# Performance work log

Measured on AMD Instinct MI355X. Metric: run time of the kernel, lower is better.

The kernel has to match this reference:

```python
import jax, jax.numpy as jnp
import numpy as np

G = 3040      # number of drugs / graph nodes in the drug-drug graph
A = 100       # atoms per molecular graph (smileNode, uniform)
TOK = 43      # token vocabulary (hard-coded in module)
FS = 75       # nfeat_smile
HS = 128      # nhid_smile
H1S = 128     # nhid1_smile
NF = 512      # nfeat (raw 384 + 128 smile emb)
NH = 256      # nhid
DH = 256      # dhid1


def setup_inputs() -> dict:
    key = jax.random.key(0)
    ks = jax.random.split(key, 20)
    s = 0.05
    inp = {
        "x": jax.random.normal(ks[0], (G, NF - H1S), dtype=jnp.float32),
        "adj_pos": jax.random.uniform(ks[1], (G, G), dtype=jnp.float32) / G,
        "adj_neg": jax.random.uniform(ks[2], (G, G), dtype=jnp.float32) / G,
        "mol_adj": jax.random.uniform(ks[3], (G, A, A), dtype=jnp.float32) / A,
        "encoded_drug": jax.random.randint(ks[4], (G, A), 0, TOK, dtype=jnp.int64),
        # learned params
        "tok_emb": jax.random.normal(ks[5], (TOK, FS), dtype=jnp.float32),
        "Wm1": jax.random.normal(ks[6], (G, FS, HS), dtype=jnp.float32) * s,
        "Wm2": jax.random.normal(ks[7], (G, HS, H1S), dtype=jnp.float32) * s,
        "Wp1": jax.random.normal(ks[8], (NF, NH), dtype=jnp.float32) * s,
        "Wp2": jax.random.normal(ks[9], (NH, NH), dtype=jnp.float32) * s,
        "Wn1": jax.random.normal(ks[10], (NF, NH), dtype=jnp.float32) * s,
        "Wn2": jax.random.normal(ks[11], (NH, NH), dtype=jnp.float32) * s,
        "Wd1": jax.random.normal(ks[12], (2 * NH, DH), dtype=jnp.float32) * s,
        "Wd2": jax.random.normal(ks[13], (DH, 2 * DH), dtype=jnp.float32) * s,
        "Wd3": jax.random.normal(ks[14], (2 * DH, DH), dtype=jnp.float32) * s,
        "Wdec": jax.random.normal(ks[15], (DH, DH), dtype=jnp.float32) * s,
    }
    return inp


def reference(x, adj_pos, adj_neg, mol_adj, encoded_drug, tok_emb,
              Wm1, Wm2, Wp1, Wp2, Wn1, Wn2, Wd1, Wd2, Wd3, Wdec):
    # --- calDrugSmileFeatures: batched over all 3040 per-graph GCN encoders ---
    feats = tok_emb[encoded_drug]                          # [G, A, FS] (embedding gather)
    h = jnp.einsum('gab,gaf,gfh->gbh', mol_adj, feats, Wm1)  # gc1: adj @ (x @ W1), per graph
    h = jnp.einsum('gab,gah,ghk->gbk', mol_adj, h, Wm2)      # gc2 (dropout inactive, eval)
    emb_drugs = jnp.max(h, axis=1)                          # [G, H1S] node-wise maxpool

    # --- main drug-drug graph ---
    xc = jnp.concatenate([x, emb_drugs], axis=1)            # [G, NF]
    hp = jax.nn.relu(adj_pos @ (xc @ Wp1))                  # GCNEncoder pos layer1
    zp = adj_pos @ (hp @ Wp2)                               # layer2
    hn = jax.nn.relu(adj_neg @ (xc @ Wn1))
    zn = adj_neg @ (hn @ Wn2)
    z = jnp.concatenate([zp, zn], axis=1)                   # [G, 2*NH]

    # --- DSN MLP (eval: dropout inactive) ---
    z = jax.nn.relu(z @ Wd1)
    z = jax.nn.relu(z @ Wd2)
    z = z @ Wd3                                             # [G, DH]

    # --- Bilinear decoder: z W z^T logits ---
    y_pred = (z @ Wdec) @ z.T                               # [G, G]
    return y_pred
```

## Files before the change

kernel.cpp:

```cpp
#include <hip/hip_runtime.h>
#include <cstdint>
#include <cstddef>

#define Gn   3040
#define An   100
#define TOKn 43
#define FSn  75
#define NFn  512
#define XC   384

typedef __attribute__((ext_vector_type(8))) short s16x8;
typedef __attribute__((ext_vector_type(4))) float f32x4;

__device__ __forceinline__ void split_bf16(float x, unsigned short &h, unsigned short &l)
{
  unsigned u = __float_as_uint(x);
  unsigned r = (u + 0x7fffu + ((u >> 16) & 1u)) & 0xffff0000u;
  h = (unsigned short)(r >> 16);
  float res = x - __uint_as_float(r);
  unsigned v = __float_as_uint(res);
  l = (unsigned short)((v + 0x7fffu + ((v >> 16) & 1u)) >> 16);
}

#define MFMA3(acc, ah, al, bh, bl)                                              \
  acc = __builtin_amdgcn_mfma_f32_16x16x32_bf16(ah, bh, acc, 0, 0, 0);          \
  acc = __builtin_amdgcn_mfma_f32_16x16x32_bf16(ah, bl, acc, 0, 0, 0);          \
  acc = __builtin_amdgcn_mfma_f32_16x16x32_bf16(al, bh, acc, 0, 0, 0);

__device__ __forceinline__ s16x8 tail_frag(const unsigned short* p, bool act)
{
  s16x8 f = {0,0,0,0,0,0,0,0};
  if (act) {
    uint2 v = *(const uint2*)p;
    f[0] = (short)(v.x & 0xffffu); f[1] = (short)(v.x >> 16);
    f[2] = (short)(v.y & 0xffffu); f[3] = (short)(v.y >> 16);
  }
  return f;
}

__device__ __forceinline__ void pack_split4(const f32x4 a, uint2 &ph, uint2 &pl)
{
  unsigned short h[4], l[4];
  #pragma unroll
  for (int r = 0; r < 4; ++r) split_bf16(a[r], h[r], l[r]);
  ph.x = (unsigned)h[0] | ((unsigned)h[1] << 16);
  ph.y = (unsigned)h[2] | ((unsigned)h[3] << 16);
  pl.x = (unsigned)l[0] | ((unsigned)l[1] << 16);
  pl.y = (unsigned)l[2] | ((unsigned)l[3] << 16);
}

__global__ void prep_tok_kernel(const float* __restrict__ tok_emb,
                                unsigned short* __restrict__ th,
                                unsigned short* __restrict__ tl)
{
  int i = blockIdx.x * 256 + threadIdx.x;
  if (i >= TOKn * 96) return;
  int r = i / 96, f = i % 96;
  float v = (f < FSn) ? tok_emb[r * FSn + f] : 0.f;
  unsigned short h, l;
  split_bf16(v, h, l);
  th[i] = h; tl[i] = l;
}

__global__ __launch_bounds__(512, 1) void smile_mfma_kernel(
    const float* __restrict__ mol_adj, const int* __restrict__ enc,
    const unsigned short* __restrict__ tokh, const unsigned short* __restrict__ tokl,
    const float* __restrict__ Wm1, const float* __restrict__ Wm2,
    float* __restrict__ xc)
{
  __shared__ __align__(16) unsigned short sm[74624];
  __shared__ int sTok[An];
  unsigned short* adjT_h = sm;
  unsigned short* adjT_l = sm + 10400;
  unsigned short* bufA_h = sm + 20800;
  unsigned short* bufA_l = sm + 34112;
  unsigned short* g1_h   = sm + 47424;
  unsigned short* g1_l   = sm + 61024;

  const int g = blockIdx.x;
  const int t = threadIdx.x;
  const int w = t >> 6, l = t & 63;
  const int lr = l & 15, lq = l >> 4;
  const f32x4 z4 = {0.f, 0.f, 0.f, 0.f};
  const s16x8 z8 = {0,0,0,0,0,0,0,0};

  if (t < An) sTok[t] = enc[g * An + t];

  {
    const float* adjg = mol_adj + (size_t)g * (An * An);
    for (int i = t; i < 2500; i += 512) {
      const int a = i / 25, b4 = (i % 25) * 4;
      float4 v = *(const float4*)&adjg[i * 4];
      unsigned short hh, ll;
      split_bf16(v.x, hh, ll); adjT_h[(b4+0)*104 + a] = hh; adjT_l[(b4+0)*104 + a] = ll;
      split_bf16(v.y, hh, ll); adjT_h[(b4+1)*104 + a] = hh; adjT_l[(b4+1)*104 + a] = ll;
      split_bf16(v.z, hh, ll); adjT_h[(b4+2)*104 + a] = hh; adjT_l[(b4+2)*104 + a] = ll;
      split_bf16(v.w, hh, ll); adjT_h[(b4+3)*104 + a] = hh; adjT_l[(b4+3)*104 + a] = ll;
    }
  }
  __syncthreads();

  {
    const int h = 16 * w + lr;
    const float* W1 = Wm1 + (size_t)g * (FSn * 128);
    s16x8 bh[3], bl[3];
    #pragma unroll
    for (int kc = 0; kc < 3; ++kc) {
      #pragma unroll
      for (int j = 0; j < 8; ++j) {
        int f = 32 * kc + 8 * lq + j;
        float v = (f < FSn) ? W1[f * 128 + h] : 0.f;
        unsigned short hh, ll;
        split_bf16(v, hh, ll);
        bh[kc][j] = (short)hh; bl[kc][j] = (short)ll;
      }
    }
    f32x4 acc[7];
    #pragma unroll
    for (int mi = 0; mi < 7; ++mi) acc[mi] = z4;
    #pragma unroll
    for (int mi = 0; mi < 7; ++mi) {
      const int a = 16 * mi + lr;
      const bool va = a < An;
      const int tk = va ? sTok[a] : 0;
      const unsigned short* th = tokh + tk * 96 + 8 * lq;
      const unsigned short* tl = tokl + tk * 96 + 8 * lq;
      #pragma unroll
      for (int kc = 0; kc < 3; ++kc) {
        s16x8 ah = z8, al = z8;
        if (va) { ah = *(const s16x8*)&th[32 * kc]; al = *(const s16x8*)&tl[32 * kc]; }
        MFMA3(acc[mi], ah, al, bh[kc], bl[kc]);
      }
    }
    #pragma unroll
    for (int mi = 0; mi < 7; ++mi) {
      const int a0 = 16 * mi + 4 * lq;
      if (a0 < An) {
        uint2 ph, pl;
        pack_split4(acc[mi], ph, pl);
        *(uint2*)&bufA_h[h * 104 + a0] = ph;
        *(uint2*)&bufA_l[h * 104 + a0] = pl;
      }
    }
  }
  __syncthreads();

  {
    const unsigned short* xh = &bufA_h[(16 * w + lr) * 104];
    const unsigned short* xl = &bufA_l[(16 * w + lr) * 104];
    f32x4 acc[7];
    #pragma unroll
    for (int ni = 0; ni < 7; ++ni) acc[ni] = z4;
    #pragma unroll
    for (int kc = 0; kc < 4; ++kc) {
      s16x8 ah, al;
      if (kc < 3) {
        ah = *(const s16x8*)&xh[32 * kc + 8 * lq];
        al = *(const s16x8*)&xl[32 * kc + 8 * lq];
      } else {
        ah = tail_frag(xh + 96, lq == 0);
        al = tail_frag(xl + 96, lq == 0);
      }
      #pragma unroll
      for (int ni = 0; ni < 7; ++ni) {
        const int b = 16 * ni + lr;
        const bool vb = b < An;
        s16x8 bh = z8, bl = z8;
        if (kc < 3) {
          if (vb) {
            bh = *(const s16x8*)&adjT_h[b * 104 + 32 * kc + 8 * lq];
            bl = *(const s16x8*)&adjT_l[b * 104 + 32 * kc + 8 * lq];
          }
        } else {
          bh = tail_frag(&adjT_h[b * 104 + 96], vb && lq == 0);
          bl = tail_frag(&adjT_l[b * 104 + 96], vb && lq == 0);
        }
        MFMA3(acc[ni], ah, al, bh, bl);
      }
    }
    __syncthreads();
    #pragma unroll
    for (int ni = 0; ni < 7; ++ni) {
      const int b = 16 * ni + lr;
      if (b < An) {
        uint2 ph, pl;
        pack_split4(acc[ni], ph, pl);
        *(uint2*)&g1_h[b * 136 + 16 * w + 4 * lq] = ph;
        *(uint2*)&g1_l[b * 136 + 16 * w + 4 * lq] = pl;
      }
    }
  }
  __syncthreads();

  {
    const int k2 = 16 * w + lr;
    const float* W2 = Wm2 + (size_t)g * (128 * 128);
    s16x8 bh[4], bl[4];
    #pragma unroll
    for (int kc = 0; kc < 4; ++kc) {
      #pragma unroll
      for (int j = 0; j < 8; ++j) {
        float v = W2[(32 * kc + 8 * lq + j) * 128 + k2];
        unsigned short hh, ll;
        split_bf16(v, hh, ll);
        bh[kc][j] = (short)hh; bl[kc][j] = (short)ll;
      }
    }
    f32x4 acc[7];
    #pragma unroll
    for (int mi = 0; mi < 7; ++mi) acc[mi] = z4;
    #pragma unroll
    for (int kc = 0; kc < 4; ++kc) {
      #pragma unroll
      for (int mi = 0; mi < 7; ++mi) {
        const int b = 16 * mi + lr;
        const bool vb = b < An;
        s16x8 ah = z8, al = z8;
        if (vb) {
          ah = *(const s16x8*)&g1_h[b * 136 + 32 * kc + 8 * lq];
          al = *(const s16x8*)&g1_l[b * 136 + 32 * kc + 8 * lq];
        }
        MFMA3(acc[mi], ah, al, bh[kc], bl[kc]);
      }
    }
    __syncthreads();
    #pragma unroll
    for (int mi = 0; mi < 7; ++mi) {
      const int b0 = 16 * mi + 4 * lq;
      if (b0 < An) {
        uint2 ph, pl;
        pack_split4(acc[mi], ph, pl);
        *(uint2*)&bufA_h[k2 * 104 + b0] = ph;
        *(uint2*)&bufA_l[k2 * 104 + b0] = pl;
      }
    }
  }
  __syncthreads();

  {
    const unsigned short* fh = &bufA_h[(16 * w + lr) * 104];
    const unsigned short* fl = &bufA_l[(16 * w + lr) * 104];
    f32x4 acc[7];
    #pragma unroll
    for (int ni = 0; ni < 7; ++ni) acc[ni] = z4;
    #pragma unroll
    for (int kc = 0; kc < 4; ++kc) {
      s16x8 ah, al;
      if (kc < 3) {
        ah = *(const s16x8*)&fh[32 * kc + 8 * lq];
        al = *(const s16x8*)&fl[32 * kc + 8 * lq];
      } else {
        ah = tail_frag(fh + 96, lq == 0);
        al = tail_frag(fl + 96, lq == 0);
      }
      #pragma unroll
      for (int ni = 0; ni < 7; ++ni) {
        const int b = 16 * ni + lr;
        const bool vb = b < An;
        s16x8 bh = z8, bl = z8;
        if (kc < 3) {
          if (vb) {
            bh = *(const s16x8*)&adjT_h[b * 104 + 32 * kc + 8 * lq];
            bl = *(const s16x8*)&adjT_l[b * 104 + 32 * kc + 8 * lq];
          }
        } else {
          bh = tail_frag(&adjT_h[b * 104 + 96], vb && lq == 0);
          bl = tail_frag(&adjT_l[b * 104 + 96], vb && lq == 0);
        }
        MFMA3(acc[ni], ah, al, bh, bl);
      }
    }
    float mr[4] = {-3.4e38f, -3.4e38f, -3.4e38f, -3.4e38f};
    #pragma unroll
    for (int ni = 0; ni < 7; ++ni) {
      if (16 * ni + lr < An) {
        #pragma unroll
        for (int r = 0; r < 4; ++r) mr[r] = fmaxf(mr[r], acc[ni][r]);
      }
    }
    #pragma unroll
    for (int d = 1; d < 16; d <<= 1) {
      #pragma unroll
      for (int r = 0; r < 4; ++r) mr[r] = fmaxf(mr[r], __shfl_xor(mr[r], d, 64));
    }
    if (lr == 0) {
      const int k2b = 16 * w + 4 * lq;
      #pragma unroll
      for (int r = 0; r < 4; ++r)
        xc[(size_t)g * NFn + XC + k2b + r] = mr[r];
    }
  }
}

__global__ __launch_bounds__(256, 2) void gemm64_kernel(
    const float* __restrict__ A0, const float* __restrict__ A1,
    const float* __restrict__ B0, const float* __restrict__ B1,
    float* __restrict__ C0, float* __restrict__ C1,
    int M, int N, int K, int relu)
{
  const float* A = blockIdx.z ? A1 : A0;
  const float* B = blockIdx.z ? B1 : B0;
  float*       C = blockIdx.z ? C1 : C0;

  __shared__ float As[16][68];
  __shared__ float Bs[16][68];

  const int t  = threadIdx.x;
  const int m0 = blockIdx.x * 64, n0 = blockIdx.y * 64;
  const int tx = t & 15, ty = t >> 4;
  const int am = t >> 2,  ak = (t & 3) * 4;
  const int bk = t >> 4,  bn = (t & 15) * 4;

  float acc[4][4];
  #pragma unroll
  for (int i = 0; i < 4; ++i)
    #pragma unroll
    for (int j = 0; j < 4; ++j) acc[i][j] = 0.f;

  for (int k0 = 0; k0 < K; k0 += 16) {
    float4 av = make_float4(0.f, 0.f, 0.f, 0.f);
    if (m0 + am < M) av = *(const float4*)&A[(size_t)(m0 + am) * K + k0 + ak];
    float4 bv = *(const float4*)&B[(size_t)(k0 + bk) * N + n0 + bn];
    __syncthreads();
    As[ak + 0][am] = av.x; As[ak + 1][am] = av.y;
    As[ak + 2][am] = av.z; As[ak + 3][am] = av.w;
    *(float4*)&Bs[bk][bn] = bv;
    __syncthreads();
    #pragma unroll
    for (int kk = 0; kk < 16; ++kk) {
      float4 a4 = *(const float4*)&As[kk][ty * 4];
      float4 b4 = *(const float4*)&Bs[kk][tx * 4];
      const float aa[4] = {a4.x, a4.y, a4.z, a4.w};
      const float bb[4] = {b4.x, b4.y, b4.z, b4.w};
      #pragma unroll
      for (int i = 0; i < 4; ++i)
        #pragma unroll
        for (int j = 0; j < 4; ++j)
          acc[i][j] = fmaf(aa[i], bb[j], acc[i][j]);
    }
  }
  #pragma unroll
  for (int i = 0; i < 4; ++i) {
    int m = m0 + ty * 4 + i;
    if (m < M) {
      float4 v = make_float4(acc[i][0], acc[i][1], acc[i][2], acc[i][3]);
      if (relu) {
        v.x = fmaxf(v.x, 0.f); v.y = fmaxf(v.y, 0.f);
        v.z = fmaxf(v.z, 0.f); v.w = fmaxf(v.w, 0.f);
      }
      *(float4*)&C[(size_t)m * N + n0 + tx * 4] = v;
    }
  }
}

__global__ __launch_bounds__(256) void convT_kernel(
    const float* __restrict__ S0, const float* __restrict__ S1,
    unsigned short* __restrict__ H0, unsigned short* __restrict__ L0,
    unsigned short* __restrict__ H1, unsigned short* __restrict__ L1)
{
  __shared__ float sT[32][33];
  const float* S     = blockIdx.z ? S1 : S0;
  unsigned short* H  = blockIdx.z ? H1 : H0;
  unsigned short* Lo = blockIdx.z ? L1 : L0;
  const int t  = threadIdx.x;
  const int r0 = blockIdx.x * 32;
  const int c0 = blockIdx.y * 32;
  {
    const int i = t >> 3, j0 = (t & 7) * 4;
    float4 v = *(const float4*)&S[(size_t)(r0 + i) * 256 + c0 + j0];
    sT[i][j0] = v.x; sT[i][j0+1] = v.y; sT[i][j0+2] = v.z; sT[i][j0+3] = v.w;
  }
  __syncthreads();
  {
    const int jj = t >> 3, ii0 = (t & 7) * 4;
    unsigned short h[4], lo[4];
    #pragma unroll
    for (int q = 0; q < 4; ++q) split_bf16(sT[ii0 + q][jj], h[q], lo[q]);
    ushort4 hv = make_ushort4(h[0], h[1], h[2], h[3]);
    ushort4 lv = make_ushort4(lo[0], lo[1], lo[2], lo[3]);
    *(ushort4*)&H [(size_t)(c0 + jj) * Gn + r0 + ii0] = hv;
    *(ushort4*)&Lo[(size_t)(c0 + jj) * Gn + r0 + ii0] = lv;
  }
}

template<bool SPLIT, bool BF32>
__global__ __launch_bounds__(256, 2) void mgemm_kernel(
    const float* __restrict__ A0, const float* __restrict__ A1,
    const unsigned short* __restrict__ Bh0, const unsigned short* __restrict__ Bl0,
    const unsigned short* __restrict__ Bh1, const unsigned short* __restrict__ Bl1,
    const float* __restrict__ Bf,
    float* __restrict__ C0, float* __restrict__ C1,
    int M, int N, int K)
{
  __shared__ __align__(16) unsigned short lds[16384];

  const int z = blockIdx.z;
  int pair, k0base, kend;
  if (SPLIT) {
    pair = z & 1;
    int s = z >> 1;
    k0base = s * 768;
    kend = k0base + 768; if (kend > K) kend = K;
  } else { pair = 0; k0base = 0; kend = K; }

  const float* A = pair ? A1 : A0;
  const unsigned short* Bh = pair ? Bh1 : Bh0;
  const unsigned short* Bl = pair ? Bl1 : Bl0;
  float* C;
  if (SPLIT) C = (pair ? C1 : C0) + (size_t)(z >> 1) * M * N;
  else       C = C0;

  const int t  = threadIdx.x;
  const int l  = t & 63;
  const int wv = t >> 6;
  const int wr = wv >> 1, wc = wv & 1;
  const int m0 = blockIdx.x * 128, n0 = blockIdx.y * 128;

  const int sm = (t >> 6) * 16 + (t & 15);
  const int sk = ((t >> 4) & 3) * 8;

  const f32x4 zero4 = {0.f, 0.f, 0.f, 0.f};
  f32x4 acc[4][4];
  #pragma unroll
  for (int i = 0; i < 4; ++i)
    #pragma unroll
    for (int j = 0; j < 4; ++j) acc[i][j] = zero4;

  for (int k0 = k0base; k0 < kend; k0 += 32) {
    float4 a00 = make_float4(0.f,0.f,0.f,0.f), a01 = a00, a10 = a00, a11 = a00;
    {
      const size_t base = (size_t)(m0 + sm) * K + k0 + sk;
      if (m0 + sm < M)      { a00 = *(const float4*)&A[base];
                              a01 = *(const float4*)&A[base + 4]; }
      if (m0 + sm + 64 < M) { a10 = *(const float4*)&A[base + (size_t)64 * K];
                              a11 = *(const float4*)&A[base + (size_t)64 * K + 4]; }
    }
    s16x8 b0h, b0l, b1h, b1l;
    float4 bf00, bf01, bf10, bf11;
    if (BF32) {
      bf00 = make_float4(0.f,0.f,0.f,0.f); bf01 = bf00; bf10 = bf00; bf11 = bf00;
      const size_t base = (size_t)(n0 + sm) * K + k0 + sk;
      if (n0 + sm < N)      { bf00 = *(const float4*)&Bf[base];
                              bf01 = *(const float4*)&Bf[base + 4]; }
      if (n0 + sm + 64 < N) { bf10 = *(const float4*)&Bf[base + (size_t)64 * K];
                              bf11 = *(const float4*)&Bf[base + (size_t)64 * K + 4]; }
    } else {
      const size_t base = (size_t)(n0 + sm) * K + k0 + sk;
      b0h = *(const s16x8*)&Bh[base];
      b0l = *(const s16x8*)&Bl[base];
      b1h = *(const s16x8*)&Bh[base + (size_t)64 * K];
      b1l = *(const s16x8*)&Bl[base + (size_t)64 * K];
    }

    s16x8 a0h, a0l, a1h, a1l;
    {
      const float av0[8] = {a00.x,a00.y,a00.z,a00.w,a01.x,a01.y,a01.z,a01.w};
      const float av1[8] = {a10.x,a10.y,a10.z,a10.w,a11.x,a11.y,a11.z,a11.w};
      #pragma unroll
      for (int j = 0; j < 8; ++j) {
        unsigned short hh, ll;
        split_bf16(av0[j], hh, ll); a0h[j] = (short)hh; a0l[j] = (short)ll;
        split_bf16(av1[j], hh, ll); a1h[j] = (short)hh; a1l[j] = (short)ll;
      }
    }
    if (BF32) {
      const float bv0[8] = {bf00.x,bf00.y,bf00.z,bf00.w,bf01.x,bf01.y,bf01.z,bf01.w};
      const float bv1[8] = {bf10.x,bf10.y,bf10.z,bf10.w,bf11.x,bf11.y,bf11.z,bf11.w};
      #pragma unroll
      for (int j = 0; j < 8; ++j) {
        unsigned short hh, ll;
        split_bf16(bv0[j], hh, ll); b0h[j] = (short)hh; b0l[j] = (short)ll;
        split_bf16(bv1[j], hh, ll); b1h[j] = (short)hh; b1l[j] = (short)ll;
      }
    }

    __syncthreads();
    {
      const int sl = (t & 63) * 8;
      const int c1 = t >> 6, c2 = c1 + 4;
      *(s16x8*)&lds[c1 * 512 + sl]          = a0h;
      *(s16x8*)&lds[4096 + c1 * 512 + sl]   = a0l;
      *(s16x8*)&lds[c2 * 512 + sl]          = a1h;
      *(s16x8*)&lds[4096 + c2 * 512 + sl]   = a1l;
      *(s16x8*)&lds[8192  + c1 * 512 + sl]  = b0h;
      *(s16x8*)&lds[12288 + c1 * 512 + sl]  = b0l;
      *(s16x8*)&lds[8192  + c2 * 512 + sl]  = b1h;
      *(s16x8*)&lds[12288 + c2 * 512 + sl]  = b1l;
    }
    __syncthreads();

    s16x8 vbh[4], vbl[4];
    #pragma unroll
    for (int ni = 0; ni < 4; ++ni) {
      const int c = wc * 4 + ni;
      vbh[ni] = *(const s16x8*)&lds[8192  + c * 512 + l * 8];
      vbl[ni] = *(const s16x8*)&lds[12288 + c * 512 + l * 8];
    }
    #pragma unroll
    for (int mi = 0; mi < 4; ++mi) {
      const int c = wr * 4 + mi;
      s16x8 ah = *(const s16x8*)&lds[c * 512 + l * 8];
      s16x8 al = *(const s16x8*)&lds[4096 + c * 512 + l * 8];
      #pragma unroll
      for (int ni = 0; ni < 4; ++ni) {
        acc[mi][ni] = __builtin_amdgcn_mfma_f32_16x16x32_bf16(ah, vbh[ni], acc[mi][ni], 0, 0, 0);
        acc[mi][ni] = __builtin_amdgcn_mfma_f32_16x16x32_bf16(ah, vbl[ni], acc[mi][ni], 0, 0, 0);
        acc[mi][ni] = __builtin_amdgcn_mfma_f32_16x16x32_bf16(al, vbh[ni], acc[mi][ni], 0, 0, 0);
      }
    }
  }

  #pragma unroll
  for (int mi = 0; mi < 4; ++mi) {
    const int rowb = m0 + (wr * 4 + mi) * 16 + (l >> 4) * 4;
    #pragma unroll
    for (int ni = 0; ni < 4; ++ni) {
      const int col = n0 + (wc * 4 + ni) * 16 + (l & 15);
      if (col < N) {
        #pragma unroll
        for (int r = 0; r < 4; ++r) {
          const int row = rowb + r;
          if (row < M) C[(size_t)row * N + col] = acc[mi][ni][r];
        }
      }
    }
  }
}

__global__ void reduce_kernel(const float* __restrict__ part, float* __restrict__ dst,
                              int S, int M, int N, int ldc, int coff, int relu)
{
  int i = blockIdx.x * blockDim.x + threadIdx.x;
  int total = M * (N / 4);
  if (i >= total) return;
  int r = i / (N / 4), c = (i % (N / 4)) * 4;
  float4 s = make_float4(0.f, 0.f, 0.f, 0.f);
  for (int j = 0; j < S; ++j) {
    float4 v = *(const float4*)&part[(size_t)j * M * N + (size_t)r * N + c];
    s.x += v.x; s.y += v.y; s.z += v.z; s.w += v.w;
  }
  if (relu) {
    s.x = fmaxf(s.x, 0.f); s.y = fmaxf(s.y, 0.f);
    s.z = fmaxf(s.z, 0.f); s.w = fmaxf(s.w, 0.f);
  }
  *(float4*)&dst[(size_t)r * ldc + coff + c] = s;
}

__global__ void copyx_kernel(const float* __restrict__ x, float* __restrict__ xc)
{
  int i = blockIdx.x * blockDim.x + threadIdx.x;
  int total = Gn * (XC / 4);
  if (i >= total) return;
  int r = i / (XC / 4), c = (i % (XC / 4)) * 4;
  *(float4*)&xc[(size_t)r * NFn + c] = *(const float4*)&x[(size_t)r * XC + c];
}

extern "C" void kernel_launch(void* const* d_in, const int* in_sizes, int n_in,
                              void* d_out, int out_size, void* d_ws, size_t ws_size,
                              hipStream_t stream)
{
  const float* x       = (const float*)d_in[0];
  const float* adj_pos = (const float*)d_in[1];
  const float* adj_neg = (const float*)d_in[2];
  const float* mol_adj = (const float*)d_in[3];
  const int*   enc     = (const int*)d_in[4];
  const float* tok_emb = (const float*)d_in[5];
  const float* Wm1     = (const float*)d_in[6];
  const float* Wm2     = (const float*)d_in[7];
  const float* Wp1     = (const float*)d_in[8];
  const float* Wp2     = (const float*)d_in[9];
  const float* Wn1     = (const float*)d_in[10];
  const float* Wn2     = (const float*)d_in[11];
  const float* Wd1     = (const float*)d_in[12];
  const float* Wd2     = (const float*)d_in[13];
  const float* Wd3     = (const float*)d_in[14];
  const float* Wdec    = (const float*)d_in[15];
  float* out = (float*)d_out;
  float* ws  = (float*)d_ws;

  const size_t MN  = (size_t)Gn * 256;
  const size_t MN2 = (size_t)Gn * 512;
  size_t o = 0;
  float* xc    = ws + o; o += MN2;
  float* P1    = ws + o; o += MN;
  float* N1    = ws + o; o += MN;
  float* hp    = ws + o; o += MN;
  float* hn    = ws + o; o += MN;
  float* P2    = ws + o; o += MN;
  float* N2    = ws + o; o += MN;
  float* zbuf  = ws + o; o += MN2;
  float* d1    = ws + o; o += MN;
  float* d2    = ws + o; o += MN2;
  float* z3    = ws + o; o += MN;
  float* tb    = ws + o; o += MN;
  float* partP = ws + o; o += 4 * MN;
  float* partN = ws + o; o += 4 * MN;
  unsigned short* tokh = (unsigned short*)(ws + o);
  unsigned short* tokl = tokh + TOKn * 96; o += 4128;

  unsigned short* BTPh = (unsigned short*)d2;
  unsigned short* BTPl = BTPh + (size_t)256 * Gn;
  unsigned short* BTNh = BTPh + (size_t)2 * 256 * Gn;
  unsigned short* BTNl = BTPh + (size_t)3 * 256 * Gn;

  dim3 b256(256);

  prep_tok_kernel<<<dim3((TOKn * 96 + 255) / 256), b256, 0, stream>>>(tok_emb, tokh, tokl);
  copyx_kernel<<<dim3((Gn * (XC / 4) + 255) / 256), b256, 0, stream>>>(x, xc);
  smile_mfma_kernel<<<dim3(Gn), dim3(512), 0, stream>>>(
      mol_adj, enc, tokh, tokl, Wm1, Wm2, xc);
  gemm64_kernel<<<dim3(48, 4, 2), b256, 0, stream>>>(xc, xc, Wp1, Wn1, P1, N1, Gn, 256, 512, 0);
  convT_kernel<<<dim3(95, 8, 2), b256, 0, stream>>>(P1, N1, BTPh, BTPl, BTNh, BTNl);
  mgemm_kernel<true, false><<<dim3(24, 2, 8), b256, 0, stream>>>(
      adj_pos, adj_neg, BTPh, BTPl, BTNh, BTNl, (const float*)nullptr,
      partP, partN, Gn, 256, Gn);
  reduce_kernel<<<dim3(760), b256, 0, stream>>>(partP, hp, 4, Gn, 256, 256, 0, 1);
  reduce_kernel<<<dim3(760), b256, 0, stream>>>(partN, hn, 4, Gn, 256, 256, 0, 1);
  gemm64_kernel<<<dim3(48, 4, 2), b256, 0, stream>>>(hp, hn, Wp2, Wn2, P2, N2, Gn, 256, 256, 0);
  convT_kernel<<<dim3(95, 8, 2), b256, 0, stream>>>(P2, N2, BTPh, BTPl, BTNh, BTNl);
  mgemm_kernel<true, false><<<dim3(24, 2, 8), b256, 0, stream>>>(
      adj_pos, adj_neg, BTPh, BTPl, BTNh, BTNl, (const float*)nullptr,
      partP, partN, Gn, 256, Gn);
  reduce_kernel<<<dim3(760), b256, 0, stream>>>(partP, zbuf, 4, Gn, 256, 512, 0, 0);
  reduce_kernel<<<dim3(760), b256, 0, stream>>>(partN, zbuf, 4, Gn, 256, 512, 256, 0);
  gemm64_kernel<<<dim3(48, 4, 1), b256, 0, stream>>>(zbuf, zbuf, Wd1, Wd1, d1, d1, Gn, 256, 512, 1);
  gemm64_kernel<<<dim3(48, 8, 1), b256, 0, stream>>>(d1, d1, Wd2, Wd2, d2, d2, Gn, 512, 256, 1);
  gemm64_kernel<<<dim3(48, 4, 1), b256, 0, stream>>>(d2, d2, Wd3, Wd3, z3, z3, Gn, 256, 512, 0);
  gemm64_kernel<<<dim3(48, 4, 1), b256, 0, stream>>>(z3, z3, Wdec, Wdec, tb, tb, Gn, 256, 256, 0);
  mgemm_kernel<false, true><<<dim3(24, 24, 1), b256, 0, stream>>>(
      tb, tb, (const unsigned short*)nullptr, (const unsigned short*)nullptr,
      (const unsigned short*)nullptr, (const unsigned short*)nullptr,
      z3, out, out, Gn, Gn, 256);
}
```

Before: 975.3 us.

## Prefetch all per-graph global loads upfront and transpose adjacency via LDS staging

```diff
diff --git a/kernel.cpp b/kernel.cpp
--- a/kernel.cpp
+++ b/kernel.cpp
@@ -69,13 +69,13 @@
     float* __restrict__ xc)
 {
   __shared__ __align__(16) unsigned short sm[74624];
-  __shared__ int sTok[An];
   unsigned short* adjT_h = sm;
   unsigned short* adjT_l = sm + 10400;
   unsigned short* bufA_h = sm + 20800;
   unsigned short* bufA_l = sm + 34112;
   unsigned short* g1_h   = sm + 47424;
   unsigned short* g1_l   = sm + 61024;
+  float* Sf = (float*)(sm + 20800);
 
   const int g = blockIdx.x;
   const int t = threadIdx.x;
@@ -84,51 +84,86 @@
   const f32x4 z4 = {0.f, 0.f, 0.f, 0.f};
   const s16x8 z8 = {0,0,0,0,0,0,0,0};
 
-  if (t < An) sTok[t] = enc[g * An + t];
+  const float* adjg = mol_adj + (size_t)g * (An * An);
+  float4 av[5];
+  #pragma unroll
+  for (int j = 0; j < 5; ++j) {
+    const int i = t + 512 * j;
+    av[j] = make_float4(0.f, 0.f, 0.f, 0.f);
+    if (i < 2500) av[j] = *(const float4*)&adjg[i * 4];
+  }
+  const int hcol = 16 * w + lr;
+  const float* W1 = Wm1 + (size_t)g * (FSn * 128);
+  float w1r[3][8];
+  #pragma unroll
+  for (int kc = 0; kc < 3; ++kc)
+    #pragma unroll
+    for (int j = 0; j < 8; ++j) {
+      const int f = 32 * kc + 8 * lq + j;
+      w1r[kc][j] = (f < FSn) ? W1[f * 128 + hcol] : 0.f;
+    }
+  const float* W2 = Wm2 + (size_t)g * (128 * 128);
+  float w2r[4][8];
+  #pragma unroll
+  for (int kc = 0; kc < 4; ++kc)
+    #pragma unroll
+    for (int j = 0; j < 8; ++j)
+      w2r[kc][j] = W2[(32 * kc + 8 * lq + j) * 128 + hcol];
+  int tkid[7];
+  #pragma unroll
+  for (int mi = 0; mi < 7; ++mi) {
+    const int a = 16 * mi + lr;
+    tkid[mi] = (a < An) ? enc[g * An + a] : 0;
+  }
+
+  #pragma unroll
+  for (int j = 0; j < 5; ++j) {
+    const int i = t + 512 * j;
+    if (i < 2500) {
+      const int a = i / 25, c4 = (i % 25) * 4;
+      float* p = &Sf[a * 101 + c4];
+      p[0] = av[j].x; p[1] = av[j].y; p[2] = av[j].z; p[3] = av[j].w;
+    }
+  }
+  __syncthreads();
+
+  #pragma unroll
+  for (int j = 0; j < 5; ++j) {
+    const int i = t + 512 * j;
+    if (i < 2500) {
+      const int b = i / 25, a4 = (i % 25) * 4;
+      f32x4 v;
+      #pragma unroll
+      for (int q = 0; q < 4; ++q) v[q] = Sf[(a4 + q) * 101 + b];
+      uint2 ph, pl;
+      pack_split4(v, ph, pl);
+      *(uint2*)&adjT_h[b * 104 + a4] = ph;
+      *(uint2*)&adjT_l[b * 104 + a4] = pl;
+    }
+  }
+  __syncthreads();
 
   {
-    const float* adjg = mol_adj + (size_t)g * (An * An);
-    for (int i = t; i < 2500; i += 512) {
-      const int a = i / 25, b4 = (i % 25) * 4;
-      float4 v = *(const float4*)&adjg[i * 4];
-      unsigned short hh, ll;
-      split_bf16(v.x, hh, ll); adjT_h[(b4+0)*104 + a] = hh; adjT_l[(b4+0)*104 + a] = ll;
-      split_bf16(v.y, hh, ll); adjT_h[(b4+1)*104 + a] = hh; adjT_l[(b4+1)*104 + a] = ll;
-      split_bf16(v.z, hh, ll); adjT_h[(b4+2)*104 + a] = hh; adjT_l[(b4+2)*104 + a] = ll;
-      split_bf16(v.w, hh, ll); adjT_h[(b4+3)*104 + a] = hh; adjT_l[(b4+3)*104 + a] = ll;
-    }
-  }
-  __syncthreads();
-
-  {
-    const int h = 16 * w + lr;
-    const float* W1 = Wm1 + (size_t)g * (FSn * 128);
     s16x8 bh[3], bl[3];
     #pragma unroll
-    for (int kc = 0; kc < 3; ++kc) {
+    for (int kc = 0; kc < 3; ++kc)
       #pragma unroll
       for (int j = 0; j < 8; ++j) {
-        int f = 32 * kc + 8 * lq + j;
-        float v = (f < FSn) ? W1[f * 128 + h] : 0.f;
         unsigned short hh, ll;
-        split_bf16(v, hh, ll);
+        split_bf16(w1r[kc][j], hh, ll);
         bh[kc][j] = (short)hh; bl[kc][j] = (short)ll;
       }
-    }
     f32x4 acc[7];
     #pragma unroll
     for (int mi = 0; mi < 7; ++mi) acc[mi] = z4;
     #pragma unroll
     for (int mi = 0; mi < 7; ++mi) {
-      const int a = 16 * mi + lr;
-      const bool va = a < An;
-      const int tk = va ? sTok[a] : 0;
-      const unsigned short* th = tokh + tk * 96 + 8 * lq;
-      const unsigned short* tl = tokl + tk * 96 + 8 * lq;
+      const unsigned short* th = tokh + tkid[mi] * 96 + 8 * lq;
+      const unsigned short* tl = tokl + tkid[mi] * 96 + 8 * lq;
       #pragma unroll
       for (int kc = 0; kc < 3; ++kc) {
-        s16x8 ah = z8, al = z8;
-        if (va) { ah = *(const s16x8*)&th[32 * kc]; al = *(const s16x8*)&tl[32 * kc]; }
+        s16x8 ah = *(const s16x8*)&th[32 * kc];
+        s16x8 al = *(const s16x8*)&tl[32 * kc];
         MFMA3(acc[mi], ah, al, bh[kc], bl[kc]);
       }
     }
@@ -138,16 +173,16 @@
       if (a0 < An) {
         uint2 ph, pl;
         pack_split4(acc[mi], ph, pl);
-        *(uint2*)&bufA_h[h * 104 + a0] = ph;
-        *(uint2*)&bufA_l[h * 104 + a0] = pl;
+        *(uint2*)&bufA_h[hcol * 104 + a0] = ph;
+        *(uint2*)&bufA_l[hcol * 104 + a0] = pl;
       }
     }
   }
   __syncthreads();
 
   {
-    const unsigned short* xh = &bufA_h[(16 * w + lr) * 104];
-    const unsigned short* xl = &bufA_l[(16 * w + lr) * 104];
+    const unsigned short* xh = &bufA_h[hcol * 104];
+    const unsigned short* xl = &bufA_l[hcol * 104];
     f32x4 acc[7];
     #pragma unroll
     for (int ni = 0; ni < 7; ++ni) acc[ni] = z4;
@@ -193,19 +228,15 @@
   __syncthreads();
 
   {
-    const int k2 = 16 * w + lr;
-    const float* W2 = Wm2 + (size_t)g * (128 * 128);
     s16x8 bh[4], bl[4];
     #pragma unroll
-    for (int kc = 0; kc < 4; ++kc) {
+    for (int kc = 0; kc < 4; ++kc)
       #pragma unroll
       for (int j = 0; j < 8; ++j) {
-        float v = W2[(32 * kc + 8 * lq + j) * 128 + k2];
         unsigned short hh, ll;
-        split_bf16(v, hh, ll);
+        split_bf16(w2r[kc][j], hh, ll);
         bh[kc][j] = (short)hh; bl[kc][j] = (short)ll;
       }
-    }
     f32x4 acc[7];
     #pragma unroll
     for (int mi = 0; mi < 7; ++mi) acc[mi] = z4;
@@ -230,16 +261,16 @@
       if (b0 < An) {
         uint2 ph, pl;
         pack_split4(acc[mi], ph, pl);
-        *(uint2*)&bufA_h[k2 * 104 + b0] = ph;
-        *(uint2*)&bufA_l[k2 * 104 + b0] = pl;
+        *(uint2*)&bufA_h[hcol * 104 + b0] = ph;
+        *(uint2*)&bufA_l[hcol * 104 + b0] = pl;
       }
     }
   }
   __syncthreads();
 
   {
-    const unsigned short* fh = &bufA_h[(16 * w + lr) * 104];
-    const unsigned short* fl = &bufA_l[(16 * w + lr) * 104];
+    const unsigned short* fh = &bufA_h[hcol * 104];
+    const unsigned short* fl = &bufA_l[hcol * 104];
     f32x4 acc[7];
     #pragma unroll
     for (int ni = 0; ni < 7; ++ni) acc[ni] = z4;
```

New measurement: 990.2 us. No clear change (+1.5%).
